# Performance work log

Measured on AMD Instinct MI355X. Metric: run time of the kernel, lower is better.

Reference implementation:

```python
import jax, jax.numpy as jnp
import numpy as np

N = 100000      # nodes
E = 1600000     # edges (avg degree 16)
IN = 128        # in_channels
OUT = 64        # out_channels
HID = 2 * OUT   # hidden = 2*out_channels


def setup_inputs() -> dict:
    key = jax.random.key(0)
    ks = jax.random.split(key, 9)
    x = jax.random.normal(ks[0], (N, IN), jnp.float32)
    edge_index = jax.random.randint(ks[1], (2, E), 0, N, jnp.int32)
    init_dist = jax.random.normal(ks[2], (N, OUT), jnp.float32)
    # GCNConv weights (glorot-ish scale) and biases
    W1 = jax.random.normal(ks[3], (IN, HID), jnp.float32) * (1.0 / np.sqrt(IN))
    b1 = jnp.zeros((HID,), jnp.float32)
    Wmu = jax.random.normal(ks[4], (HID, OUT), jnp.float32) * (1.0 / np.sqrt(HID))
    bmu = jnp.zeros((OUT,), jnp.float32)
    Wls = jax.random.normal(ks[5], (HID, OUT), jnp.float32) * (1.0 / np.sqrt(HID))
    bls = jnp.zeros((OUT,), jnp.float32)
    return {"x": x, "edge_index": edge_index, "init_dist": init_dist,
            "W1": W1, "b1": b1, "Wmu": Wmu, "bmu": bmu, "Wls": Wls, "bls": bls}


def _gcn(h, src, dst, norm, W, b, n):
    # dense transform, then normalized scatter-add aggregation over edges
    h = h @ W                               # [N, F]
    msg = h[src] * norm[:, None]            # gather + scale  [E', F]
    out = jax.ops.segment_sum(msg, dst, num_segments=n)
    return out + b


def reference(x, edge_index, init_dist, W1, b1, Wmu, bmu, Wls, bls):
    n = x.shape[0]
    # add self-loops (PyG GCNConv default)
    loops = jnp.arange(n, dtype=edge_index.dtype)
    src = jnp.concatenate([edge_index[0], loops])
    dst = jnp.concatenate([edge_index[1], loops])
    # symmetric normalization: deg over A+I, norm_e = d_src^-1/2 * d_dst^-1/2
    deg = jax.ops.segment_sum(jnp.ones_like(dst, dtype=x.dtype), dst, num_segments=n)
    dinv = jax.lax.rsqrt(jnp.maximum(deg, 1.0))  # deg >= 1 thanks to self-loops
    norm = dinv[src] * dinv[dst]

    h = _gcn(x, src, dst, norm, W1, b1, n)       # conv1 (no activation in source)
    mu = _gcn(h, src, dst, norm, Wmu, bmu, n)
    logstd = _gcn(h, src, dst, norm, Wls, bls, n)
    # reparametrize: mu + init_dist * exp(logstd)
    return mu + init_dist * jnp.exp(logstd)
```

## Files before the change

kernel.cpp:

```cpp
#include <hip/hip_runtime.h>
#include <hip/hip_bf16.h>
#include <math.h>

#define NN 100000
#define NE 1600000
#define SLOTS 48
#define NODES_PER_BUCKET 12500
#define SEGS 256
#define QUADS (NE / 4)
#define QPS ((QUADS + SEGS - 1) / SEGS)

__device__ __forceinline__ float bf2f(unsigned int u) {
    union { unsigned int u; float f; } c; c.u = u << 16; return c.f;
}
__device__ __forceinline__ unsigned short f2bf(float f) {
    union { float f; unsigned int u; } c; c.f = f;
    unsigned int x = c.u;
    return (unsigned short)((x + 0x7fffu + ((x >> 16) & 1u)) >> 16);
}

typedef __attribute__((ext_vector_type(8))) short short8;
typedef __attribute__((ext_vector_type(4))) float float4v;

__global__ __launch_bounds__(256) void k_count_fill_b(const int* __restrict__ ei,
        int* __restrict__ cnt, int* __restrict__ csr48) {
    int bucket = blockIdx.x & 7;
    int seg = blockIdx.x >> 3;
    int lo = bucket * NODES_PER_BUCKET, hi = lo + NODES_PER_BUCKET;
    int q1 = min((seg + 1) * QPS, QUADS);
    for (int q = seg * QPS + threadIdx.x; q < q1; q += 256) {
        int e0 = q * 4;
        int4 s = *(const int4*)(ei + e0);
        int4 d = *(const int4*)(ei + NE + e0);
        int r;
        if (d.x >= lo && d.x < hi) { r = atomicAdd(&cnt[d.x], 1); if (r < SLOTS) csr48[d.x * SLOTS + r] = s.x; }
        if (d.y >= lo && d.y < hi) { r = atomicAdd(&cnt[d.y], 1); if (r < SLOTS) csr48[d.y * SLOTS + r] = s.y; }
        if (d.z >= lo && d.z < hi) { r = atomicAdd(&cnt[d.z], 1); if (r < SLOTS) csr48[d.z * SLOTS + r] = s.z; }
        if (d.w >= lo && d.w < hi) { r = atomicAdd(&cnt[d.w], 1); if (r < SLOTS) csr48[d.w * SLOTS + r] = s.w; }
    }
}

__global__ __launch_bounds__(256) void k_prescale(const float* __restrict__ x,
        const int* __restrict__ cnt, float* __restrict__ dinv, unsigned short* __restrict__ xs) {
    int i = blockIdx.x * 256 + threadIdx.x;
    if (i >= NN * 32) return;
    int node = i >> 5, c = (i & 31) << 2;
    float d = rsqrtf((float)(cnt[node] + 1));
    if ((i & 31) == 0) dinv[node] = d;
    float4 v = *(const float4*)(x + (size_t)node * 128 + c);
    uint2 st;
    st.x = ((unsigned int)f2bf(d * v.y) << 16) | f2bf(d * v.x);
    st.y = ((unsigned int)f2bf(d * v.w) << 16) | f2bf(d * v.z);
    *(uint2*)(xs + (size_t)node * 128 + c) = st;
}

__global__ void k_wt(const float* __restrict__ W1, const float* __restrict__ Wmu,
                     const float* __restrict__ Wls,
                     unsigned short* __restrict__ W1t, unsigned short* __restrict__ W2t) {
    int idx = blockIdx.x * 256 + threadIdx.x;
    if (idx < 16384) {
        int n = idx >> 7, k = idx & 127;
        W1t[n * 128 + k] = f2bf(W1[k * 128 + n]);
    } else {
        int j = idx - 16384;
        int n = j >> 7, k = j & 127;
        float v = (n < 64) ? Wmu[k * 64 + n] : Wls[k * 64 + (n - 64)];
        W2t[n * 128 + k] = f2bf(v);
    }
}

__device__ __forceinline__ void gather_core(
    const unsigned short* __restrict__ tab,
    const int* __restrict__ csr, int base, int deg,
    int q, int l16, float* a) {
    int t = q;
    while (t + 4 < deg) {
        int s0 = csr[base + t];
        int s1 = csr[base + t + 4];
        uint4 r0 = *(const uint4*)(tab + (size_t)s0 * 128 + l16 * 8);
        uint4 r1 = *(const uint4*)(tab + (size_t)s1 * 128 + l16 * 8);
        a[0] += bf2f(r0.x & 0xffffu) + bf2f(r1.x & 0xffffu);
        a[1] += bf2f(r0.x >> 16)     + bf2f(r1.x >> 16);
        a[2] += bf2f(r0.y & 0xffffu) + bf2f(r1.y & 0xffffu);
        a[3] += bf2f(r0.y >> 16)     + bf2f(r1.y >> 16);
        a[4] += bf2f(r0.z & 0xffffu) + bf2f(r1.z & 0xffffu);
        a[5] += bf2f(r0.z >> 16)     + bf2f(r1.z >> 16);
        a[6] += bf2f(r0.w & 0xffffu) + bf2f(r1.w & 0xffffu);
        a[7] += bf2f(r0.w >> 16)     + bf2f(r1.w >> 16);
        t += 8;
    }
    while (t < deg) {
        int s = csr[base + t];
        uint4 r = *(const uint4*)(tab + (size_t)s * 128 + l16 * 8);
        a[0] += bf2f(r.x & 0xffffu); a[1] += bf2f(r.x >> 16);
        a[2] += bf2f(r.y & 0xffffu); a[3] += bf2f(r.y >> 16);
        a[4] += bf2f(r.z & 0xffffu); a[5] += bf2f(r.z >> 16);
        a[6] += bf2f(r.w & 0xffffu); a[7] += bf2f(r.w >> 16);
        t += 4;
    }
}

__global__ __launch_bounds__(256) void k_gatherA(
    const unsigned short* __restrict__ tab, const int* __restrict__ cnt,
    const int* __restrict__ csr48, const float* __restrict__ dinv,
    unsigned short* __restrict__ yout) {
    int node = blockIdx.x * 4 + (threadIdx.x >> 6);
    int lane = threadIdx.x & 63;
    int q = lane >> 4, l16 = lane & 15;
    float a[8] = {0.f, 0.f, 0.f, 0.f, 0.f, 0.f, 0.f, 0.f};
    if (q == 0) {
        uint4 p = *(const uint4*)(tab + (size_t)node * 128 + l16 * 8);
        a[0] = bf2f(p.x & 0xffffu); a[1] = bf2f(p.x >> 16);
        a[2] = bf2f(p.y & 0xffffu); a[3] = bf2f(p.y >> 16);
        a[4] = bf2f(p.z & 0xffffu); a[5] = bf2f(p.z >> 16);
        a[6] = bf2f(p.w & 0xffffu); a[7] = bf2f(p.w >> 16);
    }
    int deg = __builtin_amdgcn_readfirstlane(cnt[node]);
    if (deg > SLOTS) deg = SLOTS;
    gather_core(tab, csr48, node * SLOTS, deg, q, l16, a);
#pragma unroll
    for (int j = 0; j < 8; ++j) {
        a[j] += __shfl_xor(a[j], 16);
        a[j] += __shfl_xor(a[j], 32);
    }
    if (q == 0) {
        float di = dinv[node];
        uint4 st;
        st.x = ((unsigned int)f2bf(a[1] * di) << 16) | f2bf(a[0] * di);
        st.y = ((unsigned int)f2bf(a[3] * di) << 16) | f2bf(a[2] * di);
        st.z = ((unsigned int)f2bf(a[5] * di) << 16) | f2bf(a[4] * di);
        st.w = ((unsigned int)f2bf(a[7] * di) << 16) | f2bf(a[6] * di);
        *(uint4*)(yout + (size_t)node * 128 + l16 * 8) = st;
    }
}

__global__ __launch_bounds__(256) void k_gemm1(
    unsigned short* __restrict__ yio,
    const unsigned short* __restrict__ Bt,
    const float* __restrict__ bias,
    const float* __restrict__ dinv,
    int nrows) {
    __shared__ __align__(16) unsigned short As[64 * 136];
    int tid = threadIdx.x;
    int r0 = blockIdx.x * 64;
    for (int c = tid; c < 1024; c += 256) {
        int row = c >> 4, kc = (c & 15) << 3;
        int gr = r0 + row;
        short8 v = {0, 0, 0, 0, 0, 0, 0, 0};
        if (gr < nrows) v = *(const short8*)(yio + (size_t)gr * 128 + kc);
        *(short8*)(As + row * 136 + kc) = v;
    }
    __syncthreads();
    int lane = tid & 63, wave = tid >> 6;
    int quad = lane >> 4, l16 = lane & 15;
    int c0 = wave * 16 + l16;
    int c1 = 64 + c0;
    float4v acc[4][2];
#pragma unroll
    for (int rt = 0; rt < 4; ++rt) {
        float4v z = {0.f, 0.f, 0.f, 0.f};
        acc[rt][0] = z; acc[rt][1] = z;
    }
#pragma unroll
    for (int ks = 0; ks < 4; ++ks) {
        short8 b0 = *(const short8*)(Bt + (size_t)c0 * 128 + ks * 32 + quad * 8);
        short8 b1 = *(const short8*)(Bt + (size_t)c1 * 128 + ks * 32 + quad * 8);
        short8 af[4];
#pragma unroll
        for (int rt = 0; rt < 4; ++rt)
            af[rt] = *(const short8*)(As + (rt * 16 + l16) * 136 + ks * 32 + quad * 8);
#pragma unroll
        for (int rt = 0; rt < 4; ++rt) {
            acc[rt][0] = __builtin_amdgcn_mfma_f32_16x16x32_bf16(af[rt], b0, acc[rt][0], 0, 0, 0);
            acc[rt][1] = __builtin_amdgcn_mfma_f32_16x16x32_bf16(af[rt], b1, acc[rt][1], 0, 0, 0);
        }
    }
    float bc0 = bias[c0], bc1 = bias[c1];
#pragma unroll
    for (int rt = 0; rt < 4; ++rt)
#pragma unroll
        for (int reg = 0; reg < 4; ++reg) {
            int gr = r0 + rt * 16 + quad * 4 + reg;
            if (gr < nrows) {
                float dg = dinv[gr];
                yio[(size_t)gr * 128 + c0] = f2bf(dg * (acc[rt][0][reg] + bc0));
                yio[(size_t)gr * 128 + c1] = f2bf(dg * (acc[rt][1][reg] + bc1));
            }
        }
}

__global__ __launch_bounds__(256) void k_gemm2(
    const unsigned short* __restrict__ y2,
    const unsigned short* __restrict__ Bt,
    const float* __restrict__ bmu,
    const float* __restrict__ bls,
    const float* __restrict__ init,
    float* __restrict__ outp,
    int nrows) {
    __shared__ __align__(16) unsigned short As[64 * 136];
    int tid = threadIdx.x;
    int r0 = blockIdx.x * 64;
    for (int c = tid; c < 1024; c += 256) {
        int row = c >> 4, kc = (c & 15) << 3;
        int gr = r0 + row;
        short8 v = {0, 0, 0, 0, 0, 0, 0, 0};
        if (gr < nrows) v = *(const short8*)(y2 + (size_t)gr * 128 + kc);
        *(short8*)(As + row * 136 + kc) = v;
    }
    __syncthreads();
    int lane = tid & 63, wave = tid >> 6;
    int quad = lane >> 4, l16 = lane & 15;
    int cm = wave * 16 + l16;
    int cl = 64 + cm;
    float4v acc[4][2];
#pragma unroll
    for (int rt = 0; rt < 4; ++rt) {
        float4v z = {0.f, 0.f, 0.f, 0.f};
        acc[rt][0] = z; acc[rt][1] = z;
    }
#pragma unroll
    for (int ks = 0; ks < 4; ++ks) {
        short8 b0 = *(const short8*)(Bt + (size_t)cm * 128 + ks * 32 + quad * 8);
        short8 b1 = *(const short8*)(Bt + (size_t)cl * 128 + ks * 32 + quad * 8);
        short8 af[4];
#pragma unroll
        for (int rt = 0; rt < 4; ++rt)
            af[rt] = *(const short8*)(As + (rt * 16 + l16) * 136 + ks * 32 + quad * 8);
#pragma unroll
        for (int rt = 0; rt < 4; ++rt) {
            acc[rt][0] = __builtin_amdgcn_mfma_f32_16x16x32_bf16(af[rt], b0, acc[rt][0], 0, 0, 0);
            acc[rt][1] = __builtin_amdgcn_mfma_f32_16x16x32_bf16(af[rt], b1, acc[rt][1], 0, 0, 0);
        }
    }
    float bc_mu = bmu[cm], bc_ls = bls[cm];
#pragma unroll
    for (int rt = 0; rt < 4; ++rt)
#pragma unroll
        for (int reg = 0; reg < 4; ++reg) {
            int gr = r0 + rt * 16 + quad * 4 + reg;
            if (gr < nrows) {
                float mu = acc[rt][0][reg] + bc_mu;
                float ls = acc[rt][1][reg] + bc_ls;
                float idv = init[(size_t)gr * 64 + cm];
                outp[(size_t)gr * 64 + cm] = mu + idv * expf(ls);
            }
        }
}

extern "C" void kernel_launch(void* const* d_in, const int* in_sizes, int n_in,
                              void* d_out, int out_size, void* d_ws, size_t ws_size,
                              hipStream_t stream) {
    const float* x   = (const float*)d_in[0];
    const int*   ei  = (const int*)d_in[1];
    const float* ind = (const float*)d_in[2];
    const float* W1  = (const float*)d_in[3];
    const float* b1  = (const float*)d_in[4];
    const float* Wmu = (const float*)d_in[5];
    const float* bmu = (const float*)d_in[6];
    const float* Wls = (const float*)d_in[7];
    const float* bls = (const float*)d_in[8];
    float* outp = (float*)d_out;

    char* w = (char*)d_ws;
    auto carve = [&](size_t bytes) -> char* {
        char* p = w; w += (bytes + 255) & ~(size_t)255; return p;
    };
    int*   cnt  = (int*)carve((size_t)NN * 4);
    float* dinv = (float*)carve((size_t)NN * 4);
    unsigned short* W1t = (unsigned short*)carve(128 * 128 * 2);
    unsigned short* W2t = (unsigned short*)carve(128 * 128 * 2);
    unsigned short* xs  = (unsigned short*)carve((size_t)NN * 128 * 2);
    unsigned short* y   = (unsigned short*)carve((size_t)NN * 128 * 2);
    int* csr = (int*)carve((size_t)NN * SLOTS * 4);

    hipMemsetAsync(cnt, 0, (size_t)NN * 4, stream);
    k_wt<<<128, 256, 0, stream>>>(W1, Wmu, Wls, W1t, W2t);
    k_count_fill_b<<<8 * SEGS, 256, 0, stream>>>(ei, cnt, csr);
    k_prescale<<<(NN * 32 + 255) / 256, 256, 0, stream>>>(x, cnt, dinv, xs);
    k_gatherA<<<NN / 4, 256, 0, stream>>>(xs, cnt, csr, dinv, y);
    k_gemm1<<<(NN + 63) / 64, 256, 0, stream>>>(y, W1t, b1, dinv, NN);
    k_gatherA<<<NN / 4, 256, 0, stream>>>(y, cnt, csr, dinv, xs);
    k_gemm2<<<(NN + 63) / 64, 256, 0, stream>>>(xs, W2t, bmu, bls, ind, outp, NN);
}
```

Measured before the change: 386.8 us.

## Fold W1 into second-layer weights and drop the first GEMM via linearity

Since the first GCN layer has no activation, the two linear transforms are composed into a single 128x128 combined weight (W1·[Wmu|Wls]) computed on device. Both aggregations now run back to back on raw features, and the first GEMM kernel is removed. The propagated bias b1 is carried as a per-node scalar (the aggregated normalization sum) times b1·W2. The cnt memset is folded into the weight-prep kernel. This removes one GEMM pass and its memory round trip, at the cost of extra dinv gathers in the first aggregation and different bf16 rounding points.

Result: faster. 376.2 us (-2.7%).

```diff
diff --git a/kernel.cpp b/kernel.cpp
--- a/kernel.cpp
+++ b/kernel.cpp
@@ -1,5 +1,4 @@
 #include <hip/hip_runtime.h>
-#include <hip/hip_bf16.h>
 #include <math.h>
 
 #define NN 100000
@@ -40,6 +39,29 @@
     }
 }
 
+__global__ __launch_bounds__(256) void k_wprep(const float* __restrict__ W1,
+        const float* __restrict__ Wmu, const float* __restrict__ Wls,
+        const float* __restrict__ b1,
+        unsigned short* __restrict__ W2c, float* __restrict__ bw, int* __restrict__ cnt) {
+    int idx = blockIdx.x * 256 + threadIdx.x;
+    if (idx < 16384) {
+        int k = idx >> 7, n = idx & 127;
+        const float* Wx = (n < 64) ? (Wmu + n) : (Wls + (n - 64));
+        float s = 0.f;
+#pragma unroll 8
+        for (int m = 0; m < 128; ++m) s += W1[k * 128 + m] * Wx[(size_t)m * 64];
+        W2c[n * 128 + k] = f2bf(s);
+    } else if (idx < 16512) {
+        int n = idx - 16384;
+        const float* Wx = (n < 64) ? (Wmu + n) : (Wls + (n - 64));
+        float s = 0.f;
+        for (int m = 0; m < 128; ++m) s += b1[m] * Wx[(size_t)m * 64];
+        bw[n] = s;
+    } else {
+        for (int i = idx - 16512; i < NN; i += 24576 - 16512) cnt[i] = 0;
+    }
+}
+
 __global__ __launch_bounds__(256) void k_prescale(const float* __restrict__ x,
         const int* __restrict__ cnt, float* __restrict__ dinv, unsigned short* __restrict__ xs) {
     int i = blockIdx.x * 256 + threadIdx.x;
@@ -54,29 +76,94 @@
     *(uint2*)(xs + (size_t)node * 128 + c) = st;
 }
 
-__global__ void k_wt(const float* __restrict__ W1, const float* __restrict__ Wmu,
-                     const float* __restrict__ Wls,
-                     unsigned short* __restrict__ W1t, unsigned short* __restrict__ W2t) {
-    int idx = blockIdx.x * 256 + threadIdx.x;
-    if (idx < 16384) {
-        int n = idx >> 7, k = idx & 127;
-        W1t[n * 128 + k] = f2bf(W1[k * 128 + n]);
-    } else {
-        int j = idx - 16384;
-        int n = j >> 7, k = j & 127;
-        float v = (n < 64) ? Wmu[k * 64 + n] : Wls[k * 64 + (n - 64)];
-        W2t[n * 128 + k] = f2bf(v);
-    }
-}
-
-__device__ __forceinline__ void gather_core(
-    const unsigned short* __restrict__ tab,
-    const int* __restrict__ csr, int base, int deg,
-    int q, int l16, float* a) {
+__global__ __launch_bounds__(256) void k_gather1(
+    const unsigned short* __restrict__ tab, const int* __restrict__ cnt,
+    const int* __restrict__ csr48, const float* __restrict__ dinv,
+    unsigned short* __restrict__ yout, float* __restrict__ avec) {
+    int node = blockIdx.x * 4 + (threadIdx.x >> 6);
+    int lane = threadIdx.x & 63;
+    int q = lane >> 4, l16 = lane & 15;
+    float a[8] = {0.f, 0.f, 0.f, 0.f, 0.f, 0.f, 0.f, 0.f};
+    float asum = 0.f;
+    if (q == 0) {
+        uint4 p = *(const uint4*)(tab + (size_t)node * 128 + l16 * 8);
+        a[0] = bf2f(p.x & 0xffffu); a[1] = bf2f(p.x >> 16);
+        a[2] = bf2f(p.y & 0xffffu); a[3] = bf2f(p.y >> 16);
+        a[4] = bf2f(p.z & 0xffffu); a[5] = bf2f(p.z >> 16);
+        a[6] = bf2f(p.w & 0xffffu); a[7] = bf2f(p.w >> 16);
+    }
+    int deg = __builtin_amdgcn_readfirstlane(cnt[node]);
+    if (deg > SLOTS) deg = SLOTS;
+    int base = node * SLOTS;
     int t = q;
     while (t + 4 < deg) {
-        int s0 = csr[base + t];
-        int s1 = csr[base + t + 4];
+        int s0 = csr48[base + t];
+        int s1 = csr48[base + t + 4];
+        uint4 r0 = *(const uint4*)(tab + (size_t)s0 * 128 + l16 * 8);
+        uint4 r1 = *(const uint4*)(tab + (size_t)s1 * 128 + l16 * 8);
+        asum += dinv[s0] + dinv[s1];
+        a[0] += bf2f(r0.x & 0xffffu) + bf2f(r1.x & 0xffffu);
+        a[1] += bf2f(r0.x >> 16)     + bf2f(r1.x >> 16);
+        a[2] += bf2f(r0.y & 0xffffu) + bf2f(r1.y & 0xffffu);
+        a[3] += bf2f(r0.y >> 16)     + bf2f(r1.y >> 16);
+        a[4] += bf2f(r0.z & 0xffffu) + bf2f(r1.z & 0xffffu);
+        a[5] += bf2f(r0.z >> 16)     + bf2f(r1.z >> 16);
+        a[6] += bf2f(r0.w & 0xffffu) + bf2f(r1.w & 0xffffu);
+        a[7] += bf2f(r0.w >> 16)     + bf2f(r1.w >> 16);
+        t += 8;
+    }
+    while (t < deg) {
+        int s = csr48[base + t];
+        uint4 r = *(const uint4*)(tab + (size_t)s * 128 + l16 * 8);
+        asum += dinv[s];
+        a[0] += bf2f(r.x & 0xffffu); a[1] += bf2f(r.x >> 16);
+        a[2] += bf2f(r.y & 0xffffu); a[3] += bf2f(r.y >> 16);
+        a[4] += bf2f(r.z & 0xffffu); a[5] += bf2f(r.z >> 16);
+        a[6] += bf2f(r.w & 0xffffu); a[7] += bf2f(r.w >> 16);
+        t += 4;
+    }
+#pragma unroll
+    for (int j = 0; j < 8; ++j) {
+        a[j] += __shfl_xor(a[j], 16);
+        a[j] += __shfl_xor(a[j], 32);
+    }
+    asum += __shfl_xor(asum, 16);
+    asum += __shfl_xor(asum, 32);
+    if (q == 0) {
+        float di = dinv[node];
+        float d2 = di * di;
+        uint4 st;
+        st.x = ((unsigned int)f2bf(a[1] * d2) << 16) | f2bf(a[0] * d2);
+        st.y = ((unsigned int)f2bf(a[3] * d2) << 16) | f2bf(a[2] * d2);
+        st.z = ((unsigned int)f2bf(a[5] * d2) << 16) | f2bf(a[4] * d2);
+        st.w = ((unsigned int)f2bf(a[7] * d2) << 16) | f2bf(a[6] * d2);
+        *(uint4*)(yout + (size_t)node * 128 + l16 * 8) = st;
+        if (l16 == 0) avec[node] = di * (asum + di);
+    }
+}
+
+__global__ __launch_bounds__(256) void k_gather2(
+    const unsigned short* __restrict__ tab, const int* __restrict__ cnt,
+    const int* __restrict__ csr48, const float* __restrict__ dinv,
+    unsigned short* __restrict__ yout) {
+    int node = blockIdx.x * 4 + (threadIdx.x >> 6);
+    int lane = threadIdx.x & 63;
+    int q = lane >> 4, l16 = lane & 15;
+    float a[8] = {0.f, 0.f, 0.f, 0.f, 0.f, 0.f, 0.f, 0.f};
+    if (q == 0) {
+        uint4 p = *(const uint4*)(tab + (size_t)node * 128 + l16 * 8);
+        a[0] = bf2f(p.x & 0xffffu); a[1] = bf2f(p.x >> 16);
+        a[2] = bf2f(p.y & 0xffffu); a[3] = bf2f(p.y >> 16);
+        a[4] = bf2f(p.z & 0xffffu); a[5] = bf2f(p.z >> 16);
+        a[6] = bf2f(p.w & 0xffffu); a[7] = bf2f(p.w >> 16);
+    }
+    int deg = __builtin_amdgcn_readfirstlane(cnt[node]);
+    if (deg > SLOTS) deg = SLOTS;
+    int base = node * SLOTS;
+    int t = q;
+    while (t + 4 < deg) {
+        int s0 = csr48[base + t];
+        int s1 = csr48[base + t + 4];
         uint4 r0 = *(const uint4*)(tab + (size_t)s0 * 128 + l16 * 8);
         uint4 r1 = *(const uint4*)(tab + (size_t)s1 * 128 + l16 * 8);
         a[0] += bf2f(r0.x & 0xffffu) + bf2f(r1.x & 0xffffu);
@@ -90,7 +177,7 @@
         t += 8;
     }
     while (t < deg) {
-        int s = csr[base + t];
+        int s = csr48[base + t];
         uint4 r = *(const uint4*)(tab + (size_t)s * 128 + l16 * 8);
         a[0] += bf2f(r.x & 0xffffu); a[1] += bf2f(r.x >> 16);
         a[2] += bf2f(r.y & 0xffffu); a[3] += bf2f(r.y >> 16);
@@ -98,26 +185,6 @@
         a[6] += bf2f(r.w & 0xffffu); a[7] += bf2f(r.w >> 16);
         t += 4;
     }
-}
-
-__global__ __launch_bounds__(256) void k_gatherA(
-    const unsigned short* __restrict__ tab, const int* __restrict__ cnt,
-    const int* __restrict__ csr48, const float* __restrict__ dinv,
-    unsigned short* __restrict__ yout) {
-    int node = blockIdx.x * 4 + (threadIdx.x >> 6);
-    int lane = threadIdx.x & 63;
-    int q = lane >> 4, l16 = lane & 15;
-    float a[8] = {0.f, 0.f, 0.f, 0.f, 0.f, 0.f, 0.f, 0.f};
-    if (q == 0) {
-        uint4 p = *(const uint4*)(tab + (size_t)node * 128 + l16 * 8);
-        a[0] = bf2f(p.x & 0xffffu); a[1] = bf2f(p.x >> 16);
-        a[2] = bf2f(p.y & 0xffffu); a[3] = bf2f(p.y >> 16);
-        a[4] = bf2f(p.z & 0xffffu); a[5] = bf2f(p.z >> 16);
-        a[6] = bf2f(p.w & 0xffffu); a[7] = bf2f(p.w >> 16);
-    }
-    int deg = __builtin_amdgcn_readfirstlane(cnt[node]);
-    if (deg > SLOTS) deg = SLOTS;
-    gather_core(tab, csr48, node * SLOTS, deg, q, l16, a);
 #pragma unroll
     for (int j = 0; j < 8; ++j) {
         a[j] += __shfl_xor(a[j], 16);
@@ -134,64 +201,11 @@
     }
 }
 
-__global__ __launch_bounds__(256) void k_gemm1(
-    unsigned short* __restrict__ yio,
+__global__ __launch_bounds__(256) void k_gemmC(
+    const unsigned short* __restrict__ g2,
     const unsigned short* __restrict__ Bt,
-    const float* __restrict__ bias,
-    const float* __restrict__ dinv,
-    int nrows) {
-    __shared__ __align__(16) unsigned short As[64 * 136];
-    int tid = threadIdx.x;
-    int r0 = blockIdx.x * 64;
-    for (int c = tid; c < 1024; c += 256) {
-        int row = c >> 4, kc = (c & 15) << 3;
-        int gr = r0 + row;
-        short8 v = {0, 0, 0, 0, 0, 0, 0, 0};
-        if (gr < nrows) v = *(const short8*)(yio + (size_t)gr * 128 + kc);
-        *(short8*)(As + row * 136 + kc) = v;
-    }
-    __syncthreads();
-    int lane = tid & 63, wave = tid >> 6;
-    int quad = lane >> 4, l16 = lane & 15;
-    int c0 = wave * 16 + l16;
-    int c1 = 64 + c0;
-    float4v acc[4][2];
-#pragma unroll
-    for (int rt = 0; rt < 4; ++rt) {
-        float4v z = {0.f, 0.f, 0.f, 0.f};
-        acc[rt][0] = z; acc[rt][1] = z;
-    }
-#pragma unroll
-    for (int ks = 0; ks < 4; ++ks) {
-        short8 b0 = *(const short8*)(Bt + (size_t)c0 * 128 + ks * 32 + quad * 8);
-        short8 b1 = *(const short8*)(Bt + (size_t)c1 * 128 + ks * 32 + quad * 8);
-        short8 af[4];
-#pragma unroll
-        for (int rt = 0; rt < 4; ++rt)
-            af[rt] = *(const short8*)(As + (rt * 16 + l16) * 136 + ks * 32 + quad * 8);
-#pragma unroll
-        for (int rt = 0; rt < 4; ++rt) {
-            acc[rt][0] = __builtin_amdgcn_mfma_f32_16x16x32_bf16(af[rt], b0, acc[rt][0], 0, 0, 0);
-            acc[rt][1] = __builtin_amdgcn_mfma_f32_16x16x32_bf16(af[rt], b1, acc[rt][1], 0, 0, 0);
-        }
-    }
-    float bc0 = bias[c0], bc1 = bias[c1];
-#pragma unroll
-    for (int rt = 0; rt < 4; ++rt)
-#pragma unroll
-        for (int reg = 0; reg < 4; ++reg) {
-            int gr = r0 + rt * 16 + quad * 4 + reg;
-            if (gr < nrows) {
-                float dg = dinv[gr];
-                yio[(size_t)gr * 128 + c0] = f2bf(dg * (acc[rt][0][reg] + bc0));
-                yio[(size_t)gr * 128 + c1] = f2bf(dg * (acc[rt][1][reg] + bc1));
-            }
-        }
-}
-
-__global__ __launch_bounds__(256) void k_gemm2(
-    const unsigned short* __restrict__ y2,
-    const unsigned short* __restrict__ Bt,
+    const float* __restrict__ bw,
+    const float* __restrict__ avec,
     const float* __restrict__ bmu,
     const float* __restrict__ bls,
     const float* __restrict__ init,
@@ -204,7 +218,7 @@
         int row = c >> 4, kc = (c & 15) << 3;
         int gr = r0 + row;
         short8 v = {0, 0, 0, 0, 0, 0, 0, 0};
-        if (gr < nrows) v = *(const short8*)(y2 + (size_t)gr * 128 + kc);
+        if (gr < nrows) v = *(const short8*)(g2 + (size_t)gr * 128 + kc);
         *(short8*)(As + row * 136 + kc) = v;
     }
     __syncthreads();
@@ -233,14 +247,16 @@
         }
     }
     float bc_mu = bmu[cm], bc_ls = bls[cm];
+    float bwm = bw[cm], bwl = bw[cl];
 #pragma unroll
     for (int rt = 0; rt < 4; ++rt)
 #pragma unroll
         for (int reg = 0; reg < 4; ++reg) {
             int gr = r0 + rt * 16 + quad * 4 + reg;
             if (gr < nrows) {
-                float mu = acc[rt][0][reg] + bc_mu;
-                float ls = acc[rt][1][reg] + bc_ls;
+                float av = avec[gr];
+                float mu = acc[rt][0][reg] + av * bwm + bc_mu;
+                float ls = acc[rt][1][reg] + av * bwl + bc_ls;
                 float idv = init[(size_t)gr * 64 + cm];
                 outp[(size_t)gr * 64 + cm] = mu + idv * expf(ls);
             }
@@ -267,18 +283,17 @@
     };
     int*   cnt  = (int*)carve((size_t)NN * 4);
     float* dinv = (float*)carve((size_t)NN * 4);
-    unsigned short* W1t = (unsigned short*)carve(128 * 128 * 2);
-    unsigned short* W2t = (unsigned short*)carve(128 * 128 * 2);
+    float* avec = (float*)carve((size_t)NN * 4);
+    float* bw   = (float*)carve(128 * 4);
+    unsigned short* W2c = (unsigned short*)carve(128 * 128 * 2);
     unsigned short* xs  = (unsigned short*)carve((size_t)NN * 128 * 2);
-    unsigned short* y   = (unsigned short*)carve((size_t)NN * 128 * 2);
+    unsigned short* t1  = (unsigned short*)carve((size_t)NN * 128 * 2);
     int* csr = (int*)carve((size_t)NN * SLOTS * 4);
 
-    hipMemsetAsync(cnt, 0, (size_t)NN * 4, stream);
-    k_wt<<<128, 256, 0, stream>>>(W1, Wmu, Wls, W1t, W2t);
+    k_wprep<<<96, 256, 0, stream>>>(W1, Wmu, Wls, b1, W2c, bw, cnt);
     k_count_fill_b<<<8 * SEGS, 256, 0, stream>>>(ei, cnt, csr);
     k_prescale<<<(NN * 32 + 255) / 256, 256, 0, stream>>>(x, cnt, dinv, xs);
-    k_gatherA<<<NN / 4, 256, 0, stream>>>(xs, cnt, csr, dinv, y);
-    k_gemm1<<<(NN + 63) / 64, 256, 0, stream>>>(y, W1t, b1, dinv, NN);
-    k_gatherA<<<NN / 4, 256, 0, stream>>>(y, cnt, csr, dinv, xs);
-    k_gemm2<<<(NN + 63) / 64, 256, 0, stream>>>(xs, W2t, bmu, bls, ind, outp, NN);
-}
+    k_gather1<<<NN / 4, 256, 0, stream>>>(xs, cnt, csr, dinv, t1, avec);
+    k_gather2<<<NN / 4, 256, 0, stream>>>(t1, cnt, csr, dinv, xs);
+    k_gemmC<<<(NN + 63) / 64, 256, 0, stream>>>(xs, W2c, bw, avec, bmu, bls, ind, outp, NN);
+}
```
